# Kernel optimization log

Measured on AMD Instinct MI355X. Metric: run time of the kernel, lower is better.

Reference implementation:

```python
import jax, jax.numpy as jnp
import numpy as np


def setup_inputs() -> dict:
    key = jax.random.key(0)
    k1, k2, k3, k4, k5 = jax.random.split(key, 5)
    B, Di, Dh = 16384, 1024, 1024
    stdv = 1.0 / np.sqrt(Dh)
    return {
        "X": jax.random.normal(k1, (B, Di), dtype=jnp.float32),
        "h0": jax.random.normal(k2, (B, Dh), dtype=jnp.float32),
        "c0": jax.random.normal(k3, (B, Dh), dtype=jnp.float32),
        "U": jax.random.uniform(k4, (Di, 4 * Dh), dtype=jnp.float32, minval=-stdv, maxval=stdv),
        "W": jax.random.uniform(k5, (4 * Dh, Dh), dtype=jnp.float32, minval=-stdv, maxval=stdv),
    }


def reference(X, h0, c0, U, W):
    # Single-step LSTM cell: gates = X @ U + h0 @ W^T, split into i/f/g/o.
    Dh = h0.shape[-1]
    XU = X @ U                      # (B, 4*Dh)
    gates = XU + h0 @ W.T           # (B, 4*Dh)
    i, f, g, o = jnp.split(gates, 4, axis=-1)
    i = jax.nn.sigmoid(i)
    f = jax.nn.sigmoid(f)
    g = jnp.tanh(g)
    o = jax.nn.sigmoid(o)
    c = f * c0 + i * g              # (B, Dh)
    h = o * jnp.tanh(c)             # (B, Dh)
    return (h, c)
```

## Files before the change

kernel.cpp:

```cpp
#include <hip/hip_runtime.h>
#include <hip/hip_bf16.h>
#include <stdint.h>


typedef __bf16 bf16x8 __attribute__((ext_vector_type(8)));
typedef float f32x4 __attribute__((ext_vector_type(4)));

#define B_ROWS 16384
#define KDIM 2048
#define DH 1024
#define HC_ELEMS 16777216ull
#define NT 64

__device__ __forceinline__ unsigned short f2bf(float f) {
  unsigned u = __float_as_uint(f);
  u = (u + 0x7fffu + ((u >> 16) & 1u)) >> 16;
  return (unsigned short)u;
}

__device__ __forceinline__ float fsig(float x) {
  return __builtin_amdgcn_rcpf(1.0f + __expf(-x));
}
__device__ __forceinline__ float ftanh_(float x) {
  return 2.0f * __builtin_amdgcn_rcpf(1.0f + __expf(-2.0f * x)) - 1.0f;
}

__global__ void prep(const float* __restrict__ X, const float* __restrict__ h0,
                     const float* __restrict__ W, const float* __restrict__ U,
                     unsigned short* __restrict__ A, unsigned short* __restrict__ Bt) {
  __shared__ float tile[32][33];
  int b = blockIdx.x;
  if (b < 9216) {
    const float* src;
    unsigned short* dst;
    if (b < 8192) {
      size_t idx = ((size_t)b * 256 + threadIdx.x) * 16;
      int m = (int)(idx >> 11);
      int k = (int)(idx & 2047);
      src = (k < 1024) ? (X + (size_t)m * 1024 + k)
                       : (h0 + (size_t)m * 1024 + (k - 1024));
      dst = A + idx;
    } else {
      size_t idx = ((size_t)(b - 8192) * 256 + threadIdx.x) * 16;
      int n = (int)(idx >> 10);
      int k = (int)(idx & 1023);
      src = W + (size_t)n * 1024 + k;
      dst = Bt + (size_t)n * 2048 + 1024 + k;
    }
    float4 a = ((const float4*)src)[0];
    float4 bb = ((const float4*)src)[1];
    float4 c = ((const float4*)src)[2];
    float4 d = ((const float4*)src)[3];
    union { unsigned short u[16]; uint4 v[2]; } pk;
    pk.u[0] = f2bf(a.x); pk.u[1] = f2bf(a.y); pk.u[2] = f2bf(a.z); pk.u[3] = f2bf(a.w);
    pk.u[4] = f2bf(bb.x); pk.u[5] = f2bf(bb.y); pk.u[6] = f2bf(bb.z); pk.u[7] = f2bf(bb.w);
    pk.u[8]  = f2bf(c.x); pk.u[9]  = f2bf(c.y); pk.u[10] = f2bf(c.z); pk.u[11] = f2bf(c.w);
    pk.u[12] = f2bf(d.x); pk.u[13] = f2bf(d.y); pk.u[14] = f2bf(d.z); pk.u[15] = f2bf(d.w);
    *(uint4*)(dst) = pk.v[0];
    *(uint4*)(dst + 8) = pk.v[1];
  } else {
    int bb = b - 9216;
    int n0 = (bb & 127) * 32;
    int k0 = (bb >> 7) * 32;
    int tx = threadIdx.x & 31, ty = threadIdx.x >> 5;
    #pragma unroll
    for (int i = 0; i < 4; ++i)
      tile[ty + i * 8][tx] = U[(size_t)(k0 + ty + i * 8) * 4096 + n0 + tx];
    __syncthreads();
    int nrel = threadIdx.x >> 3;
    int kc = (threadIdx.x & 7) * 4;
    union { unsigned short u[4]; uint2 v8; } pk;
    #pragma unroll
    for (int i = 0; i < 4; ++i) pk.u[i] = f2bf(tile[kc + i][nrel]);
    *(uint2*)(Bt + (size_t)(n0 + nrel) * 2048 + k0 + kc) = pk.v8;
  }
}

__global__ __launch_bounds__(512, 2)
void lstm_gemm(const unsigned short* __restrict__ A, const unsigned short* __restrict__ Bt,
               const float* __restrict__ c0, float* __restrict__ out) {
  extern __shared__ char smem[];
  const int tid = threadIdx.x;
  const int wave = tid >> 6, lane = tid & 63;
  const int q = lane >> 4, cc = lane & 15;
  const int wm = wave >> 2, wn = wave & 3;

  const int bid = blockIdx.x;
  const int swz = (bid & 7) * 128 + (bid >> 3);
  const int m0 = (swz >> 4) * 256;
  const int j0 = (swz & 15) * 64;

  const int srow = lane >> 2;
  const int sseg = (lane & 3) ^ ((lane >> 3) & 3);
  uint32_t aoff[2], boff[2];
  #pragma unroll
  for (int u = 0; u < 2; ++u) {
    int rl = u * 128 + wave * 16 + srow;
    aoff[u] = (((uint32_t)(m0 + rl) << 11) + (uint32_t)(sseg * 8)) * 2u;
    int n = (((rl >> 4) & 3) << 10) + j0 + ((rl >> 6) << 4) + (rl & 15);
    boff[u] = (((uint32_t)n << 11) + (uint32_t)(sseg * 8)) * 2u;
  }
  const char* Ab = (const char*)A;
  const char* Bb = (const char*)Bt;

  auto stageAB = [&](int tt) {
    const int slot = tt & 3;
    #pragma unroll
    for (int u = 0; u < 2; ++u) {
      uintptr_t l = (uintptr_t)(smem + slot * 16384 + u * 8192 + wave * 1024);
      __builtin_amdgcn_global_load_lds(
          (const __attribute__((address_space(1))) void*)(uintptr_t)(Ab + (aoff[u] + (uint32_t)tt * 64u)),
          (__attribute__((address_space(3))) void*)(uint32_t)l, 16, 0, 0);
    }
    #pragma unroll
    for (int u = 0; u < 2; ++u) {
      uintptr_t l = (uintptr_t)(smem + 65536 + slot * 16384 + u * 8192 + wave * 1024);
      __builtin_amdgcn_global_load_lds(
          (const __attribute__((address_space(1))) void*)(uintptr_t)(Bb + (boff[u] + (uint32_t)tt * 64u)),
          (__attribute__((address_space(3))) void*)(uint32_t)l, 16, 0, 0);
    }
  };

  f32x4 acc[8][4];
  #pragma unroll
  for (int a = 0; a < 8; ++a)
    #pragma unroll
    for (int b = 0; b < 4; ++b)
      acc[a][b] = f32x4{0.f, 0.f, 0.f, 0.f};

  const uint32_t swzq = (uint32_t)((q ^ ((cc >> 1) & 3)) * 16);
  const uint32_t aRd = (uint32_t)((wm * 128 + cc) * 64) + swzq;
  const uint32_t bRd = 65536u + (uint32_t)((wn * 64 + cc) * 64) + swzq;

  auto readFrags = [&](bf16x8 (&fa)[8], bf16x8 (&fb)[4], int slot) {
    const char* sb = smem + slot * 16384;
    #pragma unroll
    for (int mi = 0; mi < 8; ++mi) fa[mi] = *(const bf16x8*)(sb + aRd + mi * 1024);
    #pragma unroll
    for (int ni = 0; ni < 4; ++ni) fb[ni] = *(const bf16x8*)(sb + bRd + ni * 1024);
  };
  auto domfma = [&](bf16x8 (&fa)[8], bf16x8 (&fb)[4]) {
    __builtin_amdgcn_s_setprio(1);
    #pragma unroll
    for (int mi = 0; mi < 8; ++mi)
      #pragma unroll
      for (int ni = 0; ni < 4; ++ni)
        acc[mi][ni] = __builtin_amdgcn_mfma_f32_16x16x32_bf16(fa[mi], fb[ni], acc[mi][ni], 0, 0, 0);
    __builtin_amdgcn_s_setprio(0);
  };

  stageAB(0); stageAB(1); stageAB(2);
  asm volatile("s_waitcnt vmcnt(4)" ::: "memory");
  __builtin_amdgcn_s_barrier();

  bf16x8 a0[8], b0[4], a1[8], b1[4];
  readFrags(a0, b0, 0);

  for (int t = 0; t < NT - 4; t += 2) {
    stageAB(t + 3);
    readFrags(a1, b1, (t + 1) & 3);
    domfma(a0, b0);
    asm volatile("s_waitcnt vmcnt(4)" ::: "memory");
    __builtin_amdgcn_s_barrier();
    stageAB(t + 4);
    readFrags(a0, b0, (t + 2) & 3);
    domfma(a1, b1);
    asm volatile("s_waitcnt vmcnt(4)" ::: "memory");
    __builtin_amdgcn_s_barrier();
  }
  stageAB(63);
  readFrags(a1, b1, 61 & 3);
  domfma(a0, b0);
  asm volatile("s_waitcnt vmcnt(4)" ::: "memory");
  __builtin_amdgcn_s_barrier();
  readFrags(a0, b0, 62 & 3);
  domfma(a1, b1);
  asm volatile("s_waitcnt vmcnt(0)" ::: "memory");
  __builtin_amdgcn_s_barrier();
  readFrags(a1, b1, 63 & 3);
  domfma(a0, b0);
  domfma(a1, b1);

  const int gj = j0 + wn * 16 + cc;
  #pragma unroll
  for (int mi = 0; mi < 8; ++mi) {
    #pragma unroll
    for (int r = 0; r < 4; ++r) {
      int grow = m0 + wm * 128 + mi * 16 + q * 4 + r;
      float iv = fsig(acc[mi][0][r]);
      float fv = fsig(acc[mi][1][r]);
      float gv = ftanh_(acc[mi][2][r]);
      float ov = fsig(acc[mi][3][r]);
      float c0v = c0[(size_t)grow * DH + gj];
      float cv = fv * c0v + iv * gv;
      float hv = ov * ftanh_(cv);
      out[(size_t)grow * DH + gj] = hv;
      out[HC_ELEMS + (size_t)grow * DH + gj] = cv;
    }
  }
}

extern "C" void kernel_launch(void* const* d_in, const int* in_sizes, int n_in,
                              void* d_out, int out_size, void* d_ws, size_t ws_size,
                              hipStream_t stream) {
  const float* X  = (const float*)d_in[0];
  const float* h0 = (const float*)d_in[1];
  const float* c0 = (const float*)d_in[2];
  const float* U  = (const float*)d_in[3];
  const float* W  = (const float*)d_in[4];
  float* out = (float*)d_out;

  unsigned short* Abf = (unsigned short*)d_ws;
  unsigned short* Bt  = Abf + 33554432ull;

  static bool attr_set = false;
  if (!attr_set) {
    (void)hipFuncSetAttribute(reinterpret_cast<const void*>(lstm_gemm),
                              hipFuncAttributeMaxDynamicSharedMemorySize, 131072);
    attr_set = true;
  }

  prep<<<13312, 256, 0, stream>>>(X, h0, W, U, Abf, Bt);
  lstm_gemm<<<1024, 512, 131072, stream>>>(Abf, Bt, c0, out);
}
```

Measured before the change: 546.5 us.

## Split GEMM K-step into two half-tile phases with barrier-synchronized ping-pong scheduling

Restructures the main loop so each K-step runs two phases: the lower half of the A fragments with B, then the upper half, each behind barriers and explicit lgkmcnt waits with sched_barrier. A and B global-to-LDS staging is split and interleaved between the phases, and the prefetch depth drops from three tiles to two. The fragment registers fall from two full sets to one split set, which frees VGPRs and fits a ping-pong style where waves alternate between memory and MFMA work. In exchange it adds more barriers per iteration and gives less time to hide global latency.

```diff
diff --git a/kernel.cpp b/kernel.cpp
--- a/kernel.cpp
+++ b/kernel.cpp
@@ -24,6 +24,10 @@
 __device__ __forceinline__ float ftanh_(float x) {
   return 2.0f * __builtin_amdgcn_rcpf(1.0f + __expf(-2.0f * x)) - 1.0f;
 }
+
+#define BAR __builtin_amdgcn_s_barrier()
+#define LGKM0 do { asm volatile("s_waitcnt lgkmcnt(0)" ::: "memory"); \
+                   __builtin_amdgcn_sched_barrier(0); } while (0)
 
 __global__ void prep(const float* __restrict__ X, const float* __restrict__ h0,
                      const float* __restrict__ W, const float* __restrict__ U,
@@ -103,7 +107,7 @@
   const char* Ab = (const char*)A;
   const char* Bb = (const char*)Bt;
 
-  auto stageAB = [&](int tt) {
+  auto stageA = [&](int tt) {
     const int slot = tt & 3;
     #pragma unroll
     for (int u = 0; u < 2; ++u) {
@@ -112,6 +116,9 @@
           (const __attribute__((address_space(1))) void*)(uintptr_t)(Ab + (aoff[u] + (uint32_t)tt * 64u)),
           (__attribute__((address_space(3))) void*)(uint32_t)l, 16, 0, 0);
     }
+  };
+  auto stageB = [&](int tt) {
+    const int slot = tt & 3;
     #pragma unroll
     for (int u = 0; u < 2; ++u) {
       uintptr_t l = (uintptr_t)(smem + 65536 + slot * 16384 + u * 8192 + wave * 1024);
@@ -132,54 +139,96 @@
   const uint32_t aRd = (uint32_t)((wm * 128 + cc) * 64) + swzq;
   const uint32_t bRd = 65536u + (uint32_t)((wn * 64 + cc) * 64) + swzq;
 
-  auto readFrags = [&](bf16x8 (&fa)[8], bf16x8 (&fb)[4], int slot) {
-    const char* sb = smem + slot * 16384;
-    #pragma unroll
-    for (int mi = 0; mi < 8; ++mi) fa[mi] = *(const bf16x8*)(sb + aRd + mi * 1024);
-    #pragma unroll
-    for (int ni = 0; ni < 4; ++ni) fb[ni] = *(const bf16x8*)(sb + bRd + ni * 1024);
-  };
-  auto domfma = [&](bf16x8 (&fa)[8], bf16x8 (&fb)[4]) {
-    __builtin_amdgcn_s_setprio(1);
-    #pragma unroll
-    for (int mi = 0; mi < 8; ++mi)
-      #pragma unroll
-      for (int ni = 0; ni < 4; ++ni)
-        acc[mi][ni] = __builtin_amdgcn_mfma_f32_16x16x32_bf16(fa[mi], fb[ni], acc[mi][ni], 0, 0, 0);
-    __builtin_amdgcn_s_setprio(0);
-  };
-
-  stageAB(0); stageAB(1); stageAB(2);
+  bf16x8 afLo[4], afHi[4], bfr[4];
+
+  stageA(0); stageB(0);
+  stageA(1); stageB(1);
   asm volatile("s_waitcnt vmcnt(4)" ::: "memory");
-  __builtin_amdgcn_s_barrier();
-
-  bf16x8 a0[8], b0[4], a1[8], b1[4];
-  readFrags(a0, b0, 0);
-
-  for (int t = 0; t < NT - 4; t += 2) {
-    stageAB(t + 3);
-    readFrags(a1, b1, (t + 1) & 3);
-    domfma(a0, b0);
+  BAR;
+
+  for (int t = 0; t < NT - 2; ++t) {
+    const char* sb = smem + (t & 3) * 16384;
+    #pragma unroll
+    for (int mi = 0; mi < 4; ++mi) afLo[mi] = *(const bf16x8*)(sb + aRd + mi * 1024);
+    #pragma unroll
+    for (int ni = 0; ni < 4; ++ni) bfr[ni] = *(const bf16x8*)(sb + bRd + ni * 1024);
+    stageA(t + 2);
+    BAR; LGKM0;
+    __builtin_amdgcn_s_setprio(1);
+    #pragma unroll
+    for (int mi = 0; mi < 4; ++mi)
+      #pragma unroll
+      for (int ni = 0; ni < 4; ++ni)
+        acc[mi][ni] = __builtin_amdgcn_mfma_f32_16x16x32_bf16(afLo[mi], bfr[ni], acc[mi][ni], 0, 0, 0);
+    __builtin_amdgcn_s_setprio(0);
+    BAR;
+    #pragma unroll
+    for (int mi = 0; mi < 4; ++mi) afHi[mi] = *(const bf16x8*)(sb + aRd + 4096 + mi * 1024);
+    stageB(t + 2);
     asm volatile("s_waitcnt vmcnt(4)" ::: "memory");
-    __builtin_amdgcn_s_barrier();
-    stageAB(t + 4);
-    readFrags(a0, b0, (t + 2) & 3);
-    domfma(a1, b1);
-    asm volatile("s_waitcnt vmcnt(4)" ::: "memory");
-    __builtin_amdgcn_s_barrier();
-  }
-  stageAB(63);
-  readFrags(a1, b1, 61 & 3);
-  domfma(a0, b0);
-  asm volatile("s_waitcnt vmcnt(4)" ::: "memory");
-  __builtin_amdgcn_s_barrier();
-  readFrags(a0, b0, 62 & 3);
-  domfma(a1, b1);
-  asm volatile("s_waitcnt vmcnt(0)" ::: "memory");
-  __builtin_amdgcn_s_barrier();
-  readFrags(a1, b1, 63 & 3);
-  domfma(a0, b0);
-  domfma(a1, b1);
+    BAR; LGKM0;
+    __builtin_amdgcn_s_setprio(1);
+    #pragma unroll
+    for (int mi = 0; mi < 4; ++mi)
+      #pragma unroll
+      for (int ni = 0; ni < 4; ++ni)
+        acc[4 + mi][ni] = __builtin_amdgcn_mfma_f32_16x16x32_bf16(afHi[mi], bfr[ni], acc[4 + mi][ni], 0, 0, 0);
+    __builtin_amdgcn_s_setprio(0);
+    BAR;
+  }
+  {
+    const char* sb = smem + ((NT - 2) & 3) * 16384;
+    #pragma unroll
+    for (int mi = 0; mi < 4; ++mi) afLo[mi] = *(const bf16x8*)(sb + aRd + mi * 1024);
+    #pragma unroll
+    for (int ni = 0; ni < 4; ++ni) bfr[ni] = *(const bf16x8*)(sb + bRd + ni * 1024);
+    BAR; LGKM0;
+    __builtin_amdgcn_s_setprio(1);
+    #pragma unroll
+    for (int mi = 0; mi < 4; ++mi)
+      #pragma unroll
+      for (int ni = 0; ni < 4; ++ni)
+        acc[mi][ni] = __builtin_amdgcn_mfma_f32_16x16x32_bf16(afLo[mi], bfr[ni], acc[mi][ni], 0, 0, 0);
+    __builtin_amdgcn_s_setprio(0);
+    BAR;
+    #pragma unroll
+    for (int mi = 0; mi < 4; ++mi) afHi[mi] = *(const bf16x8*)(sb + aRd + 4096 + mi * 1024);
+    asm volatile("s_waitcnt vmcnt(0)" ::: "memory");
+    BAR; LGKM0;
+    __builtin_amdgcn_s_setprio(1);
+    #pragma unroll
+    for (int mi = 0; mi < 4; ++mi)
+      #pragma unroll
+      for (int ni = 0; ni < 4; ++ni)
+        acc[4 + mi][ni] = __builtin_amdgcn_mfma_f32_16x16x32_bf16(afHi[mi], bfr[ni], acc[4 + mi][ni], 0, 0, 0);
+    __builtin_amdgcn_s_setprio(0);
+    BAR;
+  }
+  {
+    const char* sb = smem + ((NT - 1) & 3) * 16384;
+    #pragma unroll
+    for (int mi = 0; mi < 4; ++mi) afLo[mi] = *(const bf16x8*)(sb + aRd + mi * 1024);
+    #pragma unroll
+    for (int ni = 0; ni < 4; ++ni) bfr[ni] = *(const bf16x8*)(sb + bRd + ni * 1024);
+    LGKM0;
+    __builtin_amdgcn_s_setprio(1);
+    #pragma unroll
+    for (int mi = 0; mi < 4; ++mi)
+      #pragma unroll
+      for (int ni = 0; ni < 4; ++ni)
+        acc[mi][ni] = __builtin_amdgcn_mfma_f32_16x16x32_bf16(afLo[mi], bfr[ni], acc[mi][ni], 0, 0, 0);
+    __builtin_amdgcn_s_setprio(0);
+    #pragma unroll
+    for (int mi = 0; mi < 4; ++mi) afHi[mi] = *(const bf16x8*)(sb + aRd + 4096 + mi * 1024);
+    LGKM0;
+    __builtin_amdgcn_s_setprio(1);
+    #pragma unroll
+    for (int mi = 0; mi < 4; ++mi)
+      #pragma unroll
+      for (int ni = 0; ni < 4; ++ni)
+        acc[4 + mi][ni] = __builtin_amdgcn_mfma_f32_16x16x32_bf16(afHi[mi], bfr[ni], acc[4 + mi][ni], 0, 0, 0);
+    __builtin_amdgcn_s_setprio(0);
+  }
 
   const int gj = j0 + wn * 16 + cc;
   #pragma unroll
```

Result: faster. 526.5 us (-3.7%).

## Shrink GEMM tile to 256x128 with double buffering for higher occupancy

Applied to the files above, without the earlier changes.

Halves the N-tile per block (32 hidden units, so 128 gate columns) and doubles the grid to 2048 blocks. The 4-slot LDS pipeline with explicit vmcnt waits is replaced by a simple 2-slot double buffer with __syncthreads, and LDS drops to 48KB so launch bounds can ask for 4 blocks per CU. The goal is more concurrent waves to hide latency. In exchange, data reuse per block is lower, A-tile traffic doubles, and the deep software pipeline and prefetch distance are gone.

```diff
diff --git a/kernel.cpp b/kernel.cpp
--- a/kernel.cpp
+++ b/kernel.cpp
@@ -11,6 +11,7 @@
 #define DH 1024
 #define HC_ELEMS 16777216ull
 #define NT 64
+#define SLOT_BYTES 24576
 
 __device__ __forceinline__ unsigned short f2bf(float f) {
   unsigned u = __float_as_uint(f);
@@ -76,117 +77,89 @@
   }
 }
 
-__global__ __launch_bounds__(512, 2)
+__global__ __launch_bounds__(512, 4)
 void lstm_gemm(const unsigned short* __restrict__ A, const unsigned short* __restrict__ Bt,
                const float* __restrict__ c0, float* __restrict__ out) {
   extern __shared__ char smem[];
   const int tid = threadIdx.x;
   const int wave = tid >> 6, lane = tid & 63;
   const int q = lane >> 4, cc = lane & 15;
-  const int wm = wave >> 2, wn = wave & 3;
+  const int wm = wave >> 1, wn = wave & 1;
 
   const int bid = blockIdx.x;
-  const int swz = (bid & 7) * 128 + (bid >> 3);
-  const int m0 = (swz >> 4) * 256;
-  const int j0 = (swz & 15) * 64;
+  const int swz = (bid & 7) * 256 + (bid >> 3);
+  const int m0 = (swz >> 5) * 256;
+  const int j0 = (swz & 31) * 32;
 
   const int srow = lane >> 2;
   const int sseg = (lane & 3) ^ ((lane >> 3) & 3);
-  uint32_t aoff[2], boff[2];
+  uint32_t aoff[2], boff;
   #pragma unroll
   for (int u = 0; u < 2; ++u) {
     int rl = u * 128 + wave * 16 + srow;
     aoff[u] = (((uint32_t)(m0 + rl) << 11) + (uint32_t)(sseg * 8)) * 2u;
+  }
+  {
+    int rl = wave * 16 + srow;
     int n = (((rl >> 4) & 3) << 10) + j0 + ((rl >> 6) << 4) + (rl & 15);
-    boff[u] = (((uint32_t)n << 11) + (uint32_t)(sseg * 8)) * 2u;
+    boff = (((uint32_t)n << 11) + (uint32_t)(sseg * 8)) * 2u;
   }
   const char* Ab = (const char*)A;
   const char* Bb = (const char*)Bt;
 
   auto stageAB = [&](int tt) {
-    const int slot = tt & 3;
+    const uint32_t so = (uint32_t)(tt & 1) * SLOT_BYTES;
     #pragma unroll
     for (int u = 0; u < 2; ++u) {
-      uintptr_t l = (uintptr_t)(smem + slot * 16384 + u * 8192 + wave * 1024);
+      uintptr_t l = (uintptr_t)(smem + so + u * 8192 + wave * 1024);
       __builtin_amdgcn_global_load_lds(
           (const __attribute__((address_space(1))) void*)(uintptr_t)(Ab + (aoff[u] + (uint32_t)tt * 64u)),
           (__attribute__((address_space(3))) void*)(uint32_t)l, 16, 0, 0);
     }
-    #pragma unroll
-    for (int u = 0; u < 2; ++u) {
-      uintptr_t l = (uintptr_t)(smem + 65536 + slot * 16384 + u * 8192 + wave * 1024);
-      __builtin_amdgcn_global_load_lds(
-          (const __attribute__((address_space(1))) void*)(uintptr_t)(Bb + (boff[u] + (uint32_t)tt * 64u)),
-          (__attribute__((address_space(3))) void*)(uint32_t)l, 16, 0, 0);
-    }
+    uintptr_t l = (uintptr_t)(smem + so + 16384 + wave * 1024);
+    __builtin_amdgcn_global_load_lds(
+        (const __attribute__((address_space(1))) void*)(uintptr_t)(Bb + (boff + (uint32_t)tt * 64u)),
+        (__attribute__((address_space(3))) void*)(uint32_t)l, 16, 0, 0);
   };
 
-  f32x4 acc[8][4];
+  f32x4 acc[4][4];
   #pragma unroll
-  for (int a = 0; a < 8; ++a)
+  for (int a = 0; a < 4; ++a)
     #pragma unroll
     for (int b = 0; b < 4; ++b)
       acc[a][b] = f32x4{0.f, 0.f, 0.f, 0.f};
 
   const uint32_t swzq = (uint32_t)((q ^ ((cc >> 1) & 3)) * 16);
-  const uint32_t aRd = (uint32_t)((wm * 128 + cc) * 64) + swzq;
-  const uint32_t bRd = 65536u + (uint32_t)((wn * 64 + cc) * 64) + swzq;
+  const uint32_t aRd = (uint32_t)((wm * 64 + cc) * 64) + swzq;
+  const uint32_t bRd = 16384u + (uint32_t)((wn * 64 + cc) * 64) + swzq;
 
-  auto readFrags = [&](bf16x8 (&fa)[8], bf16x8 (&fb)[4], int slot) {
-    const char* sb = smem + slot * 16384;
+  stageAB(0);
+  __syncthreads();
+
+  for (int t = 0; t < NT; ++t) {
+    const char* sb = smem + (t & 1) * SLOT_BYTES;
+    if (t < NT - 1) stageAB(t + 1);
+    bf16x8 af[4], bf[4];
     #pragma unroll
-    for (int mi = 0; mi < 8; ++mi) fa[mi] = *(const bf16x8*)(sb + aRd + mi * 1024);
+    for (int mi = 0; mi < 4; ++mi) af[mi] = *(const bf16x8*)(sb + aRd + mi * 1024);
     #pragma unroll
-    for (int ni = 0; ni < 4; ++ni) fb[ni] = *(const bf16x8*)(sb + bRd + ni * 1024);
-  };
-  auto domfma = [&](bf16x8 (&fa)[8], bf16x8 (&fb)[4]) {
+    for (int ni = 0; ni < 4; ++ni) bf[ni] = *(const bf16x8*)(sb + bRd + ni * 1024);
     __builtin_amdgcn_s_setprio(1);
     #pragma unroll
-    for (int mi = 0; mi < 8; ++mi)
+    for (int mi = 0; mi < 4; ++mi)
       #pragma unroll
       for (int ni = 0; ni < 4; ++ni)
-        acc[mi][ni] = __builtin_amdgcn_mfma_f32_16x16x32_bf16(fa[mi], fb[ni], acc[mi][ni], 0, 0, 0);
+        acc[mi][ni] = __builtin_amdgcn_mfma_f32_16x16x32_bf16(af[mi], bf[ni], acc[mi][ni], 0, 0, 0);
     __builtin_amdgcn_s_setprio(0);
-  };
-
-  stageAB(0); stageAB(1); stageAB(2);
-  asm volatile("s_waitcnt vmcnt(4)" ::: "memory");
-  __builtin_amdgcn_s_barrier();
-
-  bf16x8 a0[8], b0[4], a1[8], b1[4];
-  readFrags(a0, b0, 0);
-
-  for (int t = 0; t < NT - 4; t += 2) {
-    stageAB(t + 3);
-    readFrags(a1, b1, (t + 1) & 3);
-    domfma(a0, b0);
-    asm volatile("s_waitcnt vmcnt(4)" ::: "memory");
-    __builtin_amdgcn_s_barrier();
-    stageAB(t + 4);
-    readFrags(a0, b0, (t + 2) & 3);
-    domfma(a1, b1);
-    asm volatile("s_waitcnt vmcnt(4)" ::: "memory");
-    __builtin_amdgcn_s_barrier();
+    if (t < NT - 1) __syncthreads();
   }
-  stageAB(63);
-  readFrags(a1, b1, 61 & 3);
-  domfma(a0, b0);
-  asm volatile("s_waitcnt vmcnt(4)" ::: "memory");
-  __builtin_amdgcn_s_barrier();
-  readFrags(a0, b0, 62 & 3);
-  domfma(a1, b1);
-  asm volatile("s_waitcnt vmcnt(0)" ::: "memory");
-  __builtin_amdgcn_s_barrier();
-  readFrags(a1, b1, 63 & 3);
-  domfma(a0, b0);
-  domfma(a1, b1);
 
   const int gj = j0 + wn * 16 + cc;
   #pragma unroll
-  for (int mi = 0; mi < 8; ++mi) {
+  for (int mi = 0; mi < 4; ++mi) {
     #pragma unroll
     for (int r = 0; r < 4; ++r) {
-      int grow = m0 + wm * 128 + mi * 16 + q * 4 + r;
+      int grow = m0 + wm * 64 + mi * 16 + q * 4 + r;
       float iv = fsig(acc[mi][0][r]);
       float fv = fsig(acc[mi][1][r]);
       float gv = ftanh_(acc[mi][2][r]);
@@ -216,10 +189,10 @@
   static bool attr_set = false;
   if (!attr_set) {
     (void)hipFuncSetAttribute(reinterpret_cast<const void*>(lstm_gemm),
-                              hipFuncAttributeMaxDynamicSharedMemorySize, 131072);
+                              hipFuncAttributeMaxDynamicSharedMemorySize, 49152);
     attr_set = true;
   }
 
   prep<<<13312, 256, 0, stream>>>(X, h0, W, U, Abf, Bt);
-  lstm_gemm<<<1024, 512, 131072, stream>>>(Abf, Bt, c0, out);
+  lstm_gemm<<<2048, 512, 49152, stream>>>(Abf, Bt, c0, out);
 }
```

New measurement: 560.7 us. +2.6%, slower.
